# Performance work log

Measured on AMD Instinct MI355X. Metric: run time of the kernel, lower is better.

The kernel has to match this reference:

```python
import jax, jax.numpy as jnp
import numpy as np

B, V, H = 8, 256, 128


def setup_inputs() -> dict:
    key = jax.random.key(0)
    ks = jax.random.split(key, 10)
    s = 0.02
    return {
        "h": jax.random.normal(ks[0], (B, V, H), dtype=jnp.float32),
        "e": jax.random.normal(ks[1], (B, V, V, H), dtype=jnp.float32),
        "graph": jax.random.randint(ks[2], (B, V, V), 0, 2, dtype=jnp.int32),
        "W_pre": jax.random.normal(ks[3], (H, H), dtype=jnp.float32) * s,
        "b_pre": jnp.zeros((H,), dtype=jnp.float32),
        "W_post": jax.random.normal(ks[4], (2 * H, H), dtype=jnp.float32) * s,
        "b_post": jnp.zeros((H,), dtype=jnp.float32),
        "W_skip": jax.random.normal(ks[5], (H, H), dtype=jnp.float32) * s,
        "b_skip": jnp.zeros((H,), dtype=jnp.float32),
    }


def reference(h, e, graph, W_pre, b_pre, W_post, b_post, W_skip, b_skip):
    silu = jax.nn.silu
    # pre self-interaction: (B,V,H)
    h0 = silu(h @ W_pre + b_pre)
    # conv: broadcast multiply edge features by sender node features
    # m[b,i,j,:] = e[b,i,j,:] * h0[b,j,:]
    m = e * h0[:, None, :, :]
    # masked_fill: graph==1 means NO edge -> zero out
    mask = (graph != 0)[..., None]  # (B,V,V,1)
    m = jnp.where(mask, jnp.float32(0), m)
    # max aggregation over neighbors j (dim 2), zeros included as in torch
    neigh = jnp.max(m, axis=2)  # (B,V,H)
    # concat + post self-interaction
    h_cat = jnp.concatenate([h0, neigh], axis=-1)  # (B,V,2H)
    h1 = silu(h_cat @ W_post + b_post)
    # skip interaction + final nonlinearity
    return silu(silu(h @ W_skip + b_skip) + h1)
```

## Files before the change

kernel.cpp:

```cpp
#include <hip/hip_runtime.h>
#include <math.h>

#define BV 2048
#define V_ 256
#define H_ 128

__device__ __forceinline__ float silu_f(float x) {
    return x / (1.0f + expf(-x));
}

__global__ __launch_bounds__(512) void k1_pre_skip(
    const float* __restrict__ h,
    const float* __restrict__ W_pre, const float* __restrict__ b_pre,
    const float* __restrict__ W_skip, const float* __restrict__ b_skip,
    float* __restrict__ h0ws, float* __restrict__ skipws)
{
    const int t = threadIdx.x;
    const int rbase = blockIdx.x * 8;
    __shared__ float s_h[8 * H_];
    if (t < 256) {
        reinterpret_cast<float4*>(s_h)[t] =
            reinterpret_cast<const float4*>(h + (size_t)rbase * H_)[t];
    }
    __syncthreads();

    const int c  = t & 127;
    const int r0 = (t >> 7) * 2;
    float a0[2] = {0.f, 0.f};
    float a1[2] = {0.f, 0.f};
    #pragma unroll 8
    for (int k = 0; k < H_; ++k) {
        float w0 = W_pre[k * H_ + c];
        float w1 = W_skip[k * H_ + c];
        #pragma unroll
        for (int r = 0; r < 2; ++r) {
            float hv = s_h[(r0 + r) * H_ + k];
            a0[r] += hv * w0;
            a1[r] += hv * w1;
        }
    }
    const float bp = b_pre[c], bs = b_skip[c];
    #pragma unroll
    for (int r = 0; r < 2; ++r) {
        int row = rbase + r0 + r;
        h0ws[row * H_ + c]   = silu_f(a0[r] + bp);
        skipws[row * H_ + c] = silu_f(a1[r] + bs);
    }
}

__global__ __launch_bounds__(256, 4) void k2_edge_max_post(
    const float4* __restrict__ e4,
    const int* __restrict__ graph,
    const float4* __restrict__ h04,
    const float* __restrict__ h0ws,
    const float* __restrict__ skipws,
    const float* __restrict__ W_post, const float* __restrict__ b_post,
    float* __restrict__ out)
{
    const int t  = threadIdx.x;
    const int bi = blockIdx.x;
    const int b  = bi >> 8;

    __shared__ int   s_list[V_];
    __shared__ int   s_listT[V_];
    __shared__ int   s_wcnt[4];
    __shared__ float s_red[8 * H_];
    __shared__ float s_x[2 * H_];
    __shared__ float s_part[2 * H_];

    const int  g    = graph[bi * V_ + t];
    const bool keep = (g == 0);
    unsigned long long bal = __ballot(keep);
    const int lane = t & 63;
    const int wv   = t >> 6;
    if (lane == 0) s_wcnt[wv] = __popcll(bal);
    __syncthreads();
    const int count = s_wcnt[0] + s_wcnt[1] + s_wcnt[2] + s_wcnt[3];
    int off = 0;
    for (int w = 0; w < wv; ++w) off += s_wcnt[w];
    if (keep) s_list[off + __popcll(bal & ((1ull << lane) - 1ull))] = t;
    __syncthreads();

    const int j0  = (count > 0) ? s_list[0] : 0;
    {
        const int jgT = t >> 5;
        const int itT = t & 31;
        const int idx = itT * 8 + jgT;
        s_listT[jgT * 32 + itT] = (idx < count) ? s_list[idx] : j0;
    }
    if (t < H_) s_x[t] = h0ws[bi * H_ + t];
    __syncthreads();

    const int h4 = t & 31;
    const int jg = t >> 5;
    const float4* __restrict__ ep = e4 + (size_t)bi * (V_ * 32) + h4;
    const float4* __restrict__ hp = h04 + ((size_t)(b << 8) * 32) + h4;
    const int4*   __restrict__ lt = reinterpret_cast<const int4*>(s_listT) + jg * 8;

    const int chunks = (count + 31) >> 5;
    float4 vmax = make_float4(-INFINITY, -INFINITY, -INFINITY, -INFINITY);
    #pragma unroll 2
    for (int c0 = 0; c0 < chunks; ++c0) {
        int4 j4 = lt[c0];
        float4 ea = ep[j4.x * 32];
        float4 eb = ep[j4.y * 32];
        float4 ec = ep[j4.z * 32];
        float4 ed = ep[j4.w * 32];
        float4 ha = hp[j4.x * 32];
        float4 hb = hp[j4.y * 32];
        float4 hc = hp[j4.z * 32];
        float4 hd = hp[j4.w * 32];
        vmax.x = fmaxf(vmax.x, ea.x * ha.x); vmax.y = fmaxf(vmax.y, ea.y * ha.y);
        vmax.z = fmaxf(vmax.z, ea.z * ha.z); vmax.w = fmaxf(vmax.w, ea.w * ha.w);
        vmax.x = fmaxf(vmax.x, eb.x * hb.x); vmax.y = fmaxf(vmax.y, eb.y * hb.y);
        vmax.z = fmaxf(vmax.z, eb.z * hb.z); vmax.w = fmaxf(vmax.w, eb.w * hb.w);
        vmax.x = fmaxf(vmax.x, ec.x * hc.x); vmax.y = fmaxf(vmax.y, ec.y * hc.y);
        vmax.z = fmaxf(vmax.z, ec.z * hc.z); vmax.w = fmaxf(vmax.w, ec.w * hc.w);
        vmax.x = fmaxf(vmax.x, ed.x * hd.x); vmax.y = fmaxf(vmax.y, ed.y * hd.y);
        vmax.z = fmaxf(vmax.z, ed.z * hd.z); vmax.w = fmaxf(vmax.w, ed.w * hd.w);
    }

    *reinterpret_cast<float4*>(&s_red[jg * H_ + h4 * 4]) = vmax;
    __syncthreads();
    if (t < H_) {
        float m = s_red[t];
        #pragma unroll
        for (int gg = 1; gg < 8; ++gg) m = fmaxf(m, s_red[gg * H_ + t]);
        if (count < V_) m = fmaxf(m, 0.0f);
        s_x[H_ + t] = m;
    }
    __syncthreads();

    const int c    = t & 127;
    const int half = t >> 7;
    const float* __restrict__ wp = W_post + (size_t)(half * H_) * H_ + c;
    float acc = 0.f;
    #pragma unroll 8
    for (int kk = 0; kk < H_; ++kk) {
        acc += s_x[half * H_ + kk] * wp[(size_t)kk * H_];
    }
    s_part[half * H_ + c] = acc;
    __syncthreads();
    if (t < H_) {
        float h1 = silu_f(s_part[t] + s_part[H_ + t] + b_post[t]);
        out[bi * H_ + t] = silu_f(skipws[bi * H_ + t] + h1);
    }
}

extern "C" void kernel_launch(void* const* d_in, const int* in_sizes, int n_in,
                              void* d_out, int out_size, void* d_ws, size_t ws_size,
                              hipStream_t stream)
{
    const float* h      = (const float*)d_in[0];
    const float* e      = (const float*)d_in[1];
    const int*   graph  = (const int*)  d_in[2];
    const float* W_pre  = (const float*)d_in[3];
    const float* b_pre  = (const float*)d_in[4];
    const float* W_post = (const float*)d_in[5];
    const float* b_post = (const float*)d_in[6];
    const float* W_skip = (const float*)d_in[7];
    const float* b_skip = (const float*)d_in[8];
    float* out = (float*)d_out;

    float* ws     = (float*)d_ws;
    float* h0ws   = ws;
    float* skipws = ws + BV * H_;

    k1_pre_skip<<<BV / 8, 512, 0, stream>>>(h, W_pre, b_pre, W_skip, b_skip,
                                            h0ws, skipws);
    k2_edge_max_post<<<BV, 256, 0, stream>>>((const float4*)e, graph,
                                             (const float4*)h0ws,
                                             h0ws, skipws,
                                             W_post, b_post, out);
}
```

Measured before the change: 365.1 us.

## Process two node rows per block in edge-max kernel to share W_post loads

Each block of the edge aggregation kernel now handles two consecutive destination nodes, with four 32-thread groups per node instead of eight, and half as many blocks are launched. Neighbor list compaction, the max reduction and the post matmul are restructured so that each W_post element loaded is reused for both rows. The goal is to halve redundant W_post traffic and the per-block fixed overhead. In exchange each group walks twice as many neighbor chunks, and there are fewer blocks to fill the GPU.

```diff
diff --git a/kernel.cpp b/kernel.cpp
--- a/kernel.cpp
+++ b/kernel.cpp
@@ -57,47 +57,72 @@
     const float* __restrict__ W_post, const float* __restrict__ b_post,
     float* __restrict__ out)
 {
-    const int t  = threadIdx.x;
-    const int bi = blockIdx.x;
-    const int b  = bi >> 8;
-
-    __shared__ int   s_list[V_];
-    __shared__ int   s_listT[V_];
-    __shared__ int   s_wcnt[4];
+    const int t   = threadIdx.x;
+    const int bi0 = blockIdx.x * 2;
+    const int b   = bi0 >> 8;
+
+    __shared__ int   s_list[2][V_];
+    __shared__ int   s_listT[2][V_];
+    __shared__ int   s_cnt[2][4];
     __shared__ float s_red[8 * H_];
-    __shared__ float s_x[2 * H_];
-    __shared__ float s_part[2 * H_];
-
-    const int  g    = graph[bi * V_ + t];
-    const bool keep = (g == 0);
-    unsigned long long bal = __ballot(keep);
+    __shared__ float s_x[2][2 * H_];
+    __shared__ float s_part[4 * H_];
+
     const int lane = t & 63;
     const int wv   = t >> 6;
-    if (lane == 0) s_wcnt[wv] = __popcll(bal);
-    __syncthreads();
-    const int count = s_wcnt[0] + s_wcnt[1] + s_wcnt[2] + s_wcnt[3];
-    int off = 0;
-    for (int w = 0; w < wv; ++w) off += s_wcnt[w];
-    if (keep) s_list[off + __popcll(bal & ((1ull << lane) - 1ull))] = t;
-    __syncthreads();
-
-    const int j0  = (count > 0) ? s_list[0] : 0;
-    {
-        const int jgT = t >> 5;
-        const int itT = t & 31;
-        const int idx = itT * 8 + jgT;
-        s_listT[jgT * 32 + itT] = (idx < count) ? s_list[idx] : j0;
-    }
-    if (t < H_) s_x[t] = h0ws[bi * H_ + t];
-    __syncthreads();
-
-    const int h4 = t & 31;
-    const int jg = t >> 5;
+    const int rw   = wv >> 1;
+    const int hf   = wv & 1;
+    const int jA   = hf * 128 + lane;
+    const int gA = graph[(bi0 + rw) * V_ + jA];
+    const int gB = graph[(bi0 + rw) * V_ + jA + 64];
+    const bool keepA = (gA == 0), keepB = (gB == 0);
+    unsigned long long balA = __ballot(keepA);
+    unsigned long long balB = __ballot(keepB);
+    if (lane == 0) { s_cnt[rw][hf * 2]     = __popcll(balA);
+                     s_cnt[rw][hf * 2 + 1] = __popcll(balB); }
+    {
+        const int r = t >> 7, hh = t & 127;
+        s_x[r][hh] = h0ws[(bi0 + r) * H_ + hh];
+    }
+    __syncthreads();
+
+    {
+        const int c0 = s_cnt[rw][0], c1 = s_cnt[rw][1], c2 = s_cnt[rw][2];
+        const int pre[4] = {0, c0, c0 + c1, c0 + c1 + c2};
+        const unsigned long long below = (1ull << lane) - 1ull;
+        if (keepA) s_list[rw][pre[hf * 2]     + __popcll(balA & below)] = jA;
+        if (keepB) s_list[rw][pre[hf * 2 + 1] + __popcll(balB & below)] = jA + 64;
+    }
+    __syncthreads();
+
+    {
+        const int r   = t >> 7;
+        const int q   = t & 127;
+        const int gsT = q >> 5;
+        const int it0 = q & 31;
+        const int cnt = s_cnt[r][0] + s_cnt[r][1] + s_cnt[r][2] + s_cnt[r][3];
+        const int j0  = (cnt > 0) ? s_list[r][0] : 0;
+        #pragma unroll
+        for (int rep = 0; rep < 2; ++rep) {
+            const int itT = it0 + rep * 32;
+            const int idx = itT * 4 + gsT;
+            s_listT[r][gsT * 64 + itT] = (idx < cnt) ? s_list[r][idx] : j0;
+        }
+    }
+    __syncthreads();
+
+    const int h4  = t & 31;
+    const int grp = t >> 5;
+    const int gr  = grp >> 2;
+    const int gs  = grp & 3;
+    const int bi  = bi0 + gr;
     const float4* __restrict__ ep = e4 + (size_t)bi * (V_ * 32) + h4;
     const float4* __restrict__ hp = h04 + ((size_t)(b << 8) * 32) + h4;
-    const int4*   __restrict__ lt = reinterpret_cast<const int4*>(s_listT) + jg * 8;
-
-    const int chunks = (count + 31) >> 5;
+    const int4*   __restrict__ lt =
+        reinterpret_cast<const int4*>(&s_listT[gr][0]) + gs * 16;
+    const int cnt_g  = s_cnt[gr][0] + s_cnt[gr][1] + s_cnt[gr][2] + s_cnt[gr][3];
+    const int chunks = (cnt_g + 15) >> 4;
+
     float4 vmax = make_float4(-INFINITY, -INFINITY, -INFINITY, -INFINITY);
     #pragma unroll 2
     for (int c0 = 0; c0 < chunks; ++c0) {
@@ -120,30 +145,38 @@
         vmax.z = fmaxf(vmax.z, ed.z * hd.z); vmax.w = fmaxf(vmax.w, ed.w * hd.w);
     }
 
-    *reinterpret_cast<float4*>(&s_red[jg * H_ + h4 * 4]) = vmax;
-    __syncthreads();
-    if (t < H_) {
-        float m = s_red[t];
+    *reinterpret_cast<float4*>(&s_red[grp * H_ + h4 * 4]) = vmax;
+    __syncthreads();
+    {
+        const int r = t >> 7, hh = t & 127;
+        float m = s_red[(r * 4 + 0) * H_ + hh];
         #pragma unroll
-        for (int gg = 1; gg < 8; ++gg) m = fmaxf(m, s_red[gg * H_ + t]);
-        if (count < V_) m = fmaxf(m, 0.0f);
-        s_x[H_ + t] = m;
+        for (int gg = 1; gg < 4; ++gg)
+            m = fmaxf(m, s_red[(r * 4 + gg) * H_ + hh]);
+        const int cnt = s_cnt[r][0] + s_cnt[r][1] + s_cnt[r][2] + s_cnt[r][3];
+        if (cnt < V_) m = fmaxf(m, 0.0f);
+        s_x[r][H_ + hh] = m;
     }
     __syncthreads();
 
     const int c    = t & 127;
     const int half = t >> 7;
     const float* __restrict__ wp = W_post + (size_t)(half * H_) * H_ + c;
-    float acc = 0.f;
+    float acc0 = 0.f, acc1 = 0.f;
     #pragma unroll 8
     for (int kk = 0; kk < H_; ++kk) {
-        acc += s_x[half * H_ + kk] * wp[(size_t)kk * H_];
-    }
-    s_part[half * H_ + c] = acc;
-    __syncthreads();
-    if (t < H_) {
-        float h1 = silu_f(s_part[t] + s_part[H_ + t] + b_post[t]);
-        out[bi * H_ + t] = silu_f(skipws[bi * H_ + t] + h1);
+        const float w = wp[(size_t)kk * H_];
+        acc0 += s_x[0][half * H_ + kk] * w;
+        acc1 += s_x[1][half * H_ + kk] * w;
+    }
+    s_part[(half * 2 + 0) * H_ + c] = acc0;
+    s_part[(half * 2 + 1) * H_ + c] = acc1;
+    __syncthreads();
+    {
+        const int r = t >> 7, cc = t & 127;
+        const float h1 = silu_f(s_part[(0 * 2 + r) * H_ + cc]
+                              + s_part[(1 * 2 + r) * H_ + cc] + b_post[cc]);
+        out[(bi0 + r) * H_ + cc] = silu_f(skipws[(bi0 + r) * H_ + cc] + h1);
     }
 }
 
@@ -168,8 +201,8 @@
 
     k1_pre_skip<<<BV / 8, 512, 0, stream>>>(h, W_pre, b_pre, W_skip, b_skip,
                                             h0ws, skipws);
-    k2_edge_max_post<<<BV, 256, 0, stream>>>((const float4*)e, graph,
-                                             (const float4*)h0ws,
-                                             h0ws, skipws,
-                                             W_post, b_post, out);
-}
+    k2_edge_max_post<<<BV / 2, 256, 0, stream>>>((const float4*)e, graph,
+                                                 (const float4*)h0ws,
+                                                 h0ws, skipws,
+                                                 W_post, b_post, out);
+}
```

After: 361.5 us. Within noise of the previous version (-1.0%).
